# Optimization experiments

Measured on AMD Instinct MI355X. Metric: run time of the kernel, lower is better.

The kernel has to match this reference:

```python
import jax, jax.numpy as jnp
import numpy as np

UNITS = 32
BACKBONE = 64

def lecun_tanh(x):
    return 1.7159 * jnp.tanh(0.666 * x)

def setup_inputs() -> dict:
    key = jax.random.key(0)
    ks = jax.random.split(key, 6)
    B, C, T, H, W = 4, 16, 32, 64, 64
    scale_b = 1.0 / np.sqrt(C + UNITS)
    scale_h = 1.0 / np.sqrt(BACKBONE)
    return {
        "x": jax.random.normal(ks[0], (B, C, T, H, W), jnp.float32),
        "Wb": jax.random.normal(ks[1], (BACKBONE, C + UNITS), jnp.float32) * scale_b,
        "bb": jnp.zeros((BACKBONE,), jnp.float32),
        "Wff1": jax.random.normal(ks[2], (UNITS, BACKBONE), jnp.float32) * scale_h,
        "bff1": jnp.zeros((UNITS,), jnp.float32),
        "Wff2": jax.random.normal(ks[3], (UNITS, BACKBONE), jnp.float32) * scale_h,
        "bff2": jnp.zeros((UNITS,), jnp.float32),
        "Wta": jax.random.normal(ks[4], (UNITS, BACKBONE), jnp.float32) * scale_h,
        "bta": jnp.zeros((UNITS,), jnp.float32),
        "Wtb": jax.random.normal(ks[5], (UNITS, BACKBONE), jnp.float32) * scale_h,
        "btb": jnp.zeros((UNITS,), jnp.float32),
    }

def reference(x, Wb, bb, Wff1, bff1, Wff2, bff2, Wta, bta, Wtb, btb):
    # x: (B, C, T, H, W) -> time-major (T, B, C, H, W) for the scan
    xs = jnp.transpose(x, (2, 0, 1, 3, 4))
    B, C, H, W = x.shape[0], x.shape[1], x.shape[3], x.shape[4]
    h0 = jnp.zeros((B, UNITS, H, W), x.dtype)
    ts = jnp.asarray(1.0, x.dtype)  # no timespans provided -> ts = 1.0

    def head(z, Wh, bh):  # channel-wise (1x1) linear: (B,K,H,W) -> (B,U,H,W)
        return jnp.einsum('bkhw,uk->buhw', z, Wh) + bh[None, :, None, None]

    def step(h, xt):
        z = jnp.concatenate([xt, h], axis=1)  # (B, C+U, H, W)
        z = lecun_tanh(jnp.einsum('bchw,kc->bkhw', z, Wb) + bb[None, :, None, None])
        ff1 = jnp.tanh(head(z, Wff1, bff1))
        ff2 = jnp.tanh(head(z, Wff2, bff2))
        t_a = head(z, Wta, bta)
        t_b = head(z, Wtb, btb)
        t_interp = jax.nn.sigmoid(t_a * ts + t_b)
        h_new = ff1 * (1.0 - t_interp) + t_interp * ff2
        return h_new, h_new

    _, ys = jax.lax.scan(step, h0, xs)  # ys: (T, B, U, H, W)
    # stack along dim=1 (batch_first) then permute(0,2,1,3,4) -> (B, U, T, H, W)
    return jnp.transpose(ys, (1, 2, 0, 3, 4))
```

## Files before the change

### kernel.cpp

```cpp
#include <hip/hip_runtime.h>
#include <hip/hip_bf16.h>


#define CIN      16
#define UNITS    32
#define BACKBONE 64
#define CZ       48
#define TSTEPS   32
#define HW       4096
#define NPIX     16
#define NTHREADS 256
#define KPAD     64

typedef __attribute__((ext_vector_type(8))) short  short8;
typedef __attribute__((ext_vector_type(4))) short  short4v;
typedef __attribute__((ext_vector_type(8))) __bf16 bf16x8;
typedef __attribute__((ext_vector_type(4))) float  float4v;

__device__ __forceinline__ unsigned short bf16_rne(float f) {
    unsigned u = __float_as_uint(f);
    return (unsigned short)((u + 0x7FFFu + ((u >> 16) & 1u)) >> 16);
}
__device__ __forceinline__ float bf16_tof(unsigned short h) {
    return __uint_as_float(((unsigned)h) << 16);
}
__device__ __forceinline__ float tanh_fast(float x) {
    float e = __expf(2.0f * x);
    return 1.0f - __fdividef(2.0f, e + 1.0f);
}
__device__ __forceinline__ float sigmoid_fast(float x) {
    return __fdividef(1.0f, 1.0f + __expf(-x));
}
__device__ __forceinline__ float4v mfma16(bf16x8 a, bf16x8 b, float4v c) {
    return __builtin_amdgcn_mfma_f32_16x16x32_bf16(a, b, c, 0, 0, 0);
}
__device__ __forceinline__ void split8(const float* v, bf16x8& hi, bf16x8& lo) {
    short8 sh, sl;
    #pragma unroll
    for (int j = 0; j < 8; ++j) {
        unsigned short h = bf16_rne(v[j]);
        sh[j] = (short)h;
        sl[j] = (short)bf16_rne(v[j] - bf16_tof(h));
    }
    hi = __builtin_bit_cast(bf16x8, sh);
    lo = __builtin_bit_cast(bf16x8, sl);
}
__device__ __forceinline__ int swoff(int p, int k) {
    return p * KPAD + ((((k >> 3) ^ (p & 7)) << 3) | (k & 7));
}

__global__ __launch_bounds__(NTHREADS, 4)
void cfc_mfma_kernel(const float* __restrict__ x,   const float* __restrict__ Wb,
                     const float* __restrict__ bb,
                     const float* __restrict__ Wff1, const float* __restrict__ bff1,
                     const float* __restrict__ Wff2, const float* __restrict__ bff2,
                     const float* __restrict__ Wta,  const float* __restrict__ bta,
                     const float* __restrict__ Wtb,  const float* __restrict__ btb,
                     float* __restrict__ out)
{
    __shared__ unsigned short zhi[NPIX * KPAD];
    __shared__ unsigned short ahi[NPIX * KPAD];

    const int tid  = threadIdx.x;
    const int wave = tid >> 6;
    const int lane = tid & 63;
    const int ln   = lane & 15;
    const int lq   = lane >> 4;

    const int gpix = blockIdx.x * NPIX;
    const int b    = gpix >> 12;
    const int pinb = gpix & 4095;

    const int mt = wave;
    bf16x8 Abb_hi[2], Abb_lo[2];
    #pragma unroll
    for (int kt = 0; kt < 2; ++kt) {
        float v[8];
        #pragma unroll
        for (int j = 0; j < 8; ++j) {
            int k  = kt * 32 + lq * 8 + j;
            int ki = (k < CZ) ? k : (CZ - 1);
            float raw = Wb[(mt * 16 + ln) * CZ + ki];
            v[j] = (k < CZ) ? raw : 0.0f;
        }
        split8(v, Abb_hi[kt], Abb_lo[kt]);
    }
    const int hsel = ln & 3;
    const float* Whp = (hsel == 0) ? Wff1 : (hsel == 1) ? Wff2 : (hsel == 2) ? Wta : Wtb;
    bf16x8 Ah_hi[2][2], Ah_lo[2][2];
    #pragma unroll
    for (int i = 0; i < 2; ++i) {
        const int u = (wave * 2 + i) * 4 + (ln >> 2);
        #pragma unroll
        for (int kt = 0; kt < 2; ++kt) {
            float v[8];
            #pragma unroll
            for (int j = 0; j < 8; ++j) v[j] = Whp[u * BACKBONE + kt * 32 + lq * 8 + j];
            split8(v, Ah_hi[i][kt], Ah_lo[i][kt]);
        }
    }
    float bbias[4];
    #pragma unroll
    for (int r = 0; r < 4; ++r) bbias[r] = bb[mt * 16 + lq * 4 + r];
    float hbias[2][4];
    #pragma unroll
    for (int i = 0; i < 2; ++i) {
        const int u2 = (wave * 2 + i) * 4 + lq;
        hbias[i][0] = bff1[u2]; hbias[i][1] = bff2[u2];
        hbias[i][2] = bta[u2];  hbias[i][3] = btb[u2];
    }

    for (int i = tid; i < NPIX * KPAD / 2; i += NTHREADS)
        ((unsigned*)zhi)[i] = 0u;
    __syncthreads();
    const int xc = tid >> 4;
    const int xp = tid & 15;
    const float* xb = x + (size_t)(b * CIN + xc) * (TSTEPS * HW) + pinb + xp;
    const int xoff = swoff(xp, xc);
    zhi[xoff] = bf16_rne(xb[0]);

    const int zrd0 = swoff(ln, lq * 8);
    const int zrd1 = swoff(ln, 32 + lq * 8);
    const int awr  = swoff(ln, mt * 16 + lq * 4);
    const int u0   = (wave * 2 + 0) * 4 + lq;
    const int u1   = (wave * 2 + 1) * 4 + lq;
    const int ho0  = swoff(ln, CIN + u0);
    const int ho1  = swoff(ln, CIN + u1);
    float* po0 = out + (size_t)((b * UNITS + u0) * TSTEPS) * HW + pinb + ln;
    float* po1 = out + (size_t)((b * UNITS + u1) * TSTEPS) * HW + pinb + ln;
    int xoffs = HW;
    __syncthreads();

    #pragma unroll 1
    for (int t = 0; t < TSTEPS; ++t) {
        const float xv = xb[xoffs];

        {
            bf16x8 Z0 = __builtin_bit_cast(bf16x8, *(const short8*)&zhi[zrd0]);
            bf16x8 Z1 = __builtin_bit_cast(bf16x8, *(const short8*)&zhi[zrd1]);
            float4v acc = {bbias[0], bbias[1], bbias[2], bbias[3]};
            acc = mfma16(Abb_hi[0], Z0, acc);
            acc = mfma16(Abb_lo[0], Z0, acc);
            acc = mfma16(Abb_hi[1], Z1, acc);
            acc = mfma16(Abb_lo[1], Z1, acc);
            short4v ph;
            #pragma unroll
            for (int r = 0; r < 4; ++r)
                ph[r] = (short)bf16_rne(1.7159f * tanh_fast(0.666f * acc[r]));
            *(short4v*)&ahi[awr] = ph;
        }
        __syncthreads();

        {
            bf16x8 A0 = __builtin_bit_cast(bf16x8, *(const short8*)&ahi[zrd0]);
            bf16x8 A1 = __builtin_bit_cast(bf16x8, *(const short8*)&ahi[zrd1]);

            zhi[xoff] = bf16_rne(xv);

            {
                float4v acc = {hbias[0][0], hbias[0][1], hbias[0][2], hbias[0][3]};
                acc = mfma16(Ah_hi[0][0], A0, acc);
                acc = mfma16(Ah_lo[0][0], A0, acc);
                acc = mfma16(Ah_hi[0][1], A1, acc);
                acc = mfma16(Ah_lo[0][1], A1, acc);
                float f1 = tanh_fast(acc[0]);
                float f2 = tanh_fast(acc[1]);
                float ti = sigmoid_fast(acc[2] + acc[3]);
                float hn = f1 + ti * (f2 - f1);
                *po0 = hn;  po0 += HW;
                zhi[ho0] = bf16_rne(hn);
            }
            {
                float4v acc = {hbias[1][0], hbias[1][1], hbias[1][2], hbias[1][3]};
                acc = mfma16(Ah_hi[1][0], A0, acc);
                acc = mfma16(Ah_lo[1][0], A0, acc);
                acc = mfma16(Ah_hi[1][1], A1, acc);
                acc = mfma16(Ah_lo[1][1], A1, acc);
                float f1 = tanh_fast(acc[0]);
                float f2 = tanh_fast(acc[1]);
                float ti = sigmoid_fast(acc[2] + acc[3]);
                float hn = f1 + ti * (f2 - f1);
                *po1 = hn;  po1 += HW;
                zhi[ho1] = bf16_rne(hn);
            }
        }
        __syncthreads();

        xoffs += (t < TSTEPS - 2) ? HW : 0;
    }
}

extern "C" void kernel_launch(void* const* d_in, const int* in_sizes, int n_in,
                              void* d_out, int out_size, void* d_ws, size_t ws_size,
                              hipStream_t stream) {
    dim3 grid(4 * HW / NPIX);
    cfc_mfma_kernel<<<grid, NTHREADS, 0, stream>>>(
        (const float*)d_in[0], (const float*)d_in[1], (const float*)d_in[2],
        (const float*)d_in[3], (const float*)d_in[4], (const float*)d_in[5],
        (const float*)d_in[6], (const float*)d_in[7], (const float*)d_in[8],
        (const float*)d_in[9], (const float*)d_in[10],
        (float*)d_out);
}
```

Measured before the change: 173.9 us.

## Run each 16-pixel tile in one wave, keep recurrent state in registers

The four-wave block that passed z and backbone activations through shared memory with two barriers per step becomes a single 64-lane wave per block. That wave computes all four backbone M-tiles and all eight head tiles itself. Weight rows are permuted so each MFMA's output lane layout matches the next MFMA's B-operand layout, which lets x, h and the activations move between stages entirely in registers with no LDS and no syncs. It also uses hardware exp2/rcp with packed bf16 conversion and prefetches the next timestep's x. In exchange each wave holds far more weight registers and runs four times the MFMA work serially, and occupancy is set to one block per launch-bounds hint.

```diff
diff --git a/kernel.cpp b/kernel.cpp
--- a/kernel.cpp
+++ b/kernel.cpp
@@ -9,13 +9,12 @@
 #define TSTEPS   32
 #define HW       4096
 #define NPIX     16
-#define NTHREADS 256
-#define KPAD     64
+#define NTHREADS 64
 
 typedef __attribute__((ext_vector_type(8))) short  short8;
-typedef __attribute__((ext_vector_type(4))) short  short4v;
 typedef __attribute__((ext_vector_type(8))) __bf16 bf16x8;
 typedef __attribute__((ext_vector_type(4))) float  float4v;
+typedef __attribute__((ext_vector_type(4))) unsigned int uint4v;
 
 __device__ __forceinline__ unsigned short bf16_rne(float f) {
     unsigned u = __float_as_uint(f);
@@ -24,12 +23,34 @@
 __device__ __forceinline__ float bf16_tof(unsigned short h) {
     return __uint_as_float(((unsigned)h) << 16);
 }
-__device__ __forceinline__ float tanh_fast(float x) {
-    float e = __expf(2.0f * x);
-    return 1.0f - __fdividef(2.0f, e + 1.0f);
-}
-__device__ __forceinline__ float sigmoid_fast(float x) {
-    return __fdividef(1.0f, 1.0f + __expf(-x));
+__device__ __forceinline__ unsigned cvt_pk_bf16(float lo, float hi) {
+    unsigned r;
+    asm("v_cvt_pk_bf16_f32 %0, %1, %2" : "=v"(r) : "v"(lo), "v"(hi));
+    return r;
+}
+
+#if __has_builtin(__builtin_amdgcn_exp2f)
+#define EXP2F(x) __builtin_amdgcn_exp2f(x)
+#else
+#define EXP2F(x) __expf(0.69314718056f * (x))
+#endif
+#if __has_builtin(__builtin_amdgcn_rcpf)
+#define RCPF(x) __builtin_amdgcn_rcpf(x)
+#else
+#define RCPF(x) __fdividef(1.0f, (x))
+#endif
+
+__device__ __forceinline__ float lecun_tanh_f(float v) {
+    float e = EXP2F(1.92166925f * v);
+    return fmaf(-3.4318f, RCPF(e + 1.0f), 1.7159f);
+}
+__device__ __forceinline__ float tanh_f(float v) {
+    float e = EXP2F(2.88539008f * v);
+    return fmaf(-2.0f, RCPF(e + 1.0f), 1.0f);
+}
+__device__ __forceinline__ float sigmoid_f(float v) {
+    float e = EXP2F(-1.44269504f * v);
+    return RCPF(1.0f + e);
 }
 __device__ __forceinline__ float4v mfma16(bf16x8 a, bf16x8 b, float4v c) {
     return __builtin_amdgcn_mfma_f32_16x16x32_bf16(a, b, c, 0, 0, 0);
@@ -45,11 +66,8 @@
     hi = __builtin_bit_cast(bf16x8, sh);
     lo = __builtin_bit_cast(bf16x8, sl);
 }
-__device__ __forceinline__ int swoff(int p, int k) {
-    return p * KPAD + ((((k >> 3) ^ (p & 7)) << 3) | (k & 7));
-}
-
-__global__ __launch_bounds__(NTHREADS, 4)
+
+__global__ __launch_bounds__(NTHREADS, 1)
 void cfc_mfma_kernel(const float* __restrict__ x,   const float* __restrict__ Wb,
                      const float* __restrict__ bb,
                      const float* __restrict__ Wff1, const float* __restrict__ bff1,
@@ -58,135 +76,149 @@
                      const float* __restrict__ Wtb,  const float* __restrict__ btb,
                      float* __restrict__ out)
 {
-    __shared__ unsigned short zhi[NPIX * KPAD];
-    __shared__ unsigned short ahi[NPIX * KPAD];
-
-    const int tid  = threadIdx.x;
-    const int wave = tid >> 6;
-    const int lane = tid & 63;
+    const int lane = threadIdx.x;
     const int ln   = lane & 15;
     const int lq   = lane >> 4;
 
     const int gpix = blockIdx.x * NPIX;
     const int b    = gpix >> 12;
     const int pinb = gpix & 4095;
-
-    const int mt = wave;
-    bf16x8 Abb_hi[2], Abb_lo[2];
-    #pragma unroll
-    for (int kt = 0; kt < 2; ++kt) {
-        float v[8];
-        #pragma unroll
-        for (int j = 0; j < 8; ++j) {
-            int k  = kt * 32 + lq * 8 + j;
-            int ki = (k < CZ) ? k : (CZ - 1);
-            float raw = Wb[(mt * 16 + ln) * CZ + ki];
-            v[j] = (k < CZ) ? raw : 0.0f;
-        }
-        split8(v, Abb_hi[kt], Abb_lo[kt]);
-    }
-    const int hsel = ln & 3;
-    const float* Whp = (hsel == 0) ? Wff1 : (hsel == 1) ? Wff2 : (hsel == 2) ? Wta : Wtb;
-    bf16x8 Ah_hi[2][2], Ah_lo[2][2];
-    #pragma unroll
-    for (int i = 0; i < 2; ++i) {
-        const int u = (wave * 2 + i) * 4 + (ln >> 2);
+    const int px   = pinb + ln;
+
+    bf16x8 Abb_hi[4][2], Abb_lo[4][2];
+    #pragma unroll
+    for (int mt = 0; mt < 4; ++mt) {
         #pragma unroll
         for (int kt = 0; kt < 2; ++kt) {
             float v[8];
             #pragma unroll
-            for (int j = 0; j < 8; ++j) v[j] = Whp[u * BACKBONE + kt * 32 + lq * 8 + j];
+            for (int j = 0; j < 8; ++j) {
+                int c = kt * 32 + lq * 8 + j;
+                v[j] = (c < CZ) ? Wb[(mt * 16 + ln) * CZ + c] : 0.0f;
+            }
+            split8(v, Abb_hi[mt][kt], Abb_lo[mt][kt]);
+        }
+    }
+    float bbias[4][4];
+    #pragma unroll
+    for (int mt = 0; mt < 4; ++mt)
+        #pragma unroll
+        for (int r = 0; r < 4; ++r)
+            bbias[mt][r] = bb[mt * 16 + lq * 4 + r];
+
+    const int head = ln & 3;
+    const float* Whp = (head == 0) ? Wff1 : (head == 1) ? Wff2 : (head == 2) ? Wta : Wtb;
+    const int urow = (((ln >> 2) + 2) & 3) * 8;
+    bf16x8 Ah_hi[8][2], Ah_lo[8][2];
+    #pragma unroll
+    for (int i = 0; i < 8; ++i) {
+        #pragma unroll
+        for (int kt = 0; kt < 2; ++kt) {
+            float v[8];
+            #pragma unroll
+            for (int j = 0; j < 8; ++j) {
+                int n = 32 * kt + (j >> 2) * 16 + lq * 4 + (j & 3);
+                v[j] = Whp[(urow + i) * BACKBONE + n];
+            }
             split8(v, Ah_hi[i][kt], Ah_lo[i][kt]);
         }
     }
-    float bbias[4];
-    #pragma unroll
-    for (int r = 0; r < 4; ++r) bbias[r] = bb[mt * 16 + lq * 4 + r];
-    float hbias[2][4];
-    #pragma unroll
-    for (int i = 0; i < 2; ++i) {
-        const int u2 = (wave * 2 + i) * 4 + lq;
-        hbias[i][0] = bff1[u2]; hbias[i][1] = bff2[u2];
-        hbias[i][2] = bta[u2];  hbias[i][3] = btb[u2];
-    }
-
-    for (int i = tid; i < NPIX * KPAD / 2; i += NTHREADS)
-        ((unsigned*)zhi)[i] = 0u;
-    __syncthreads();
-    const int xc = tid >> 4;
-    const int xp = tid & 15;
-    const float* xb = x + (size_t)(b * CIN + xc) * (TSTEPS * HW) + pinb + xp;
-    const int xoff = swoff(xp, xc);
-    zhi[xoff] = bf16_rne(xb[0]);
-
-    const int zrd0 = swoff(ln, lq * 8);
-    const int zrd1 = swoff(ln, 32 + lq * 8);
-    const int awr  = swoff(ln, mt * 16 + lq * 4);
-    const int u0   = (wave * 2 + 0) * 4 + lq;
-    const int u1   = (wave * 2 + 1) * 4 + lq;
-    const int ho0  = swoff(ln, CIN + u0);
-    const int ho1  = swoff(ln, CIN + u1);
-    float* po0 = out + (size_t)((b * UNITS + u0) * TSTEPS) * HW + pinb + ln;
-    float* po1 = out + (size_t)((b * UNITS + u1) * TSTEPS) * HW + pinb + ln;
-    int xoffs = HW;
-    __syncthreads();
+    const int ub = ((lq + 2) & 3) * 8;
+    float hbias[8][4];
+    #pragma unroll
+    for (int i = 0; i < 8; ++i) {
+        int u = ub + i;
+        hbias[i][0] = bff1[u]; hbias[i][1] = bff2[u];
+        hbias[i][2] = bta[u];  hbias[i][3] = btb[u];
+    }
+
+    const int cb = (lq & 1) * 8;
+    unsigned xo[8], oo[8];
+    #pragma unroll
+    for (int j = 0; j < 8; ++j)
+        xo[j] = (unsigned)(((b * CIN + cb + j) * TSTEPS) * HW + px);
+    #pragma unroll
+    for (int i = 0; i < 8; ++i)
+        oo[i] = (unsigned)(((b * UNITS + ub + i) * TSTEPS) * HW + px);
+
+    float xa[8], xb2[8];
+    #pragma unroll
+    for (int j = 0; j < 8; ++j) xa[j] = x[xo[j]];
+    unsigned hpk[4] = {0u, 0u, 0u, 0u};
+    unsigned toff = 0;
+
+    auto step = [&](int t, float (&xc)[8], float (&xn)[8]) {
+        const unsigned tn = toff + ((t < TSTEPS - 1) ? (unsigned)HW : 0u);
+        #pragma unroll
+        for (int j = 0; j < 8; ++j) xn[j] = x[xo[j] + tn];
+
+        unsigned xpk[4];
+        #pragma unroll
+        for (int p = 0; p < 4; ++p) xpk[p] = cvt_pk_bf16(xc[2 * p], xc[2 * p + 1]);
+        const bool xl = (lq < 2);
+        unsigned z0u[4], z1u[4];
+        #pragma unroll
+        for (int p = 0; p < 4; ++p) {
+            z0u[p] = xl ? xpk[p] : hpk[p];
+            z1u[p] = xl ? hpk[p] : 0u;
+        }
+        uint4v zv0 = {z0u[0], z0u[1], z0u[2], z0u[3]};
+        uint4v zv1 = {z1u[0], z1u[1], z1u[2], z1u[3]};
+        bf16x8 Z0 = __builtin_bit_cast(bf16x8, zv0);
+        bf16x8 Z1 = __builtin_bit_cast(bf16x8, zv1);
+
+        float4v acc[4];
+        #pragma unroll
+        for (int mt = 0; mt < 4; ++mt) {
+            float4v a = {bbias[mt][0], bbias[mt][1], bbias[mt][2], bbias[mt][3]};
+            a = mfma16(Abb_hi[mt][0], Z0, a);
+            a = mfma16(Abb_lo[mt][0], Z0, a);
+            a = mfma16(Abb_hi[mt][1], Z1, a);
+            a = mfma16(Abb_lo[mt][1], Z1, a);
+            acc[mt] = a;
+        }
+
+        bf16x8 A2[2];
+        #pragma unroll
+        for (int kt = 0; kt < 2; ++kt) {
+            unsigned w[4];
+            #pragma unroll
+            for (int h2 = 0; h2 < 2; ++h2) {
+                float g0 = lecun_tanh_f(acc[2 * kt + h2][0]);
+                float g1 = lecun_tanh_f(acc[2 * kt + h2][1]);
+                float g2 = lecun_tanh_f(acc[2 * kt + h2][2]);
+                float g3 = lecun_tanh_f(acc[2 * kt + h2][3]);
+                w[2 * h2 + 0] = cvt_pk_bf16(g0, g1);
+                w[2 * h2 + 1] = cvt_pk_bf16(g2, g3);
+            }
+            uint4v wv = {w[0], w[1], w[2], w[3]};
+            A2[kt] = __builtin_bit_cast(bf16x8, wv);
+        }
+
+        float hn[8];
+        #pragma unroll
+        for (int i = 0; i < 8; ++i) {
+            float4v c = {hbias[i][0], hbias[i][1], hbias[i][2], hbias[i][3]};
+            c = mfma16(Ah_hi[i][0], A2[0], c);
+            c = mfma16(Ah_lo[i][0], A2[0], c);
+            c = mfma16(Ah_hi[i][1], A2[1], c);
+            c = mfma16(Ah_lo[i][1], A2[1], c);
+            float f1 = tanh_f(c[0]);
+            float f2 = tanh_f(c[1]);
+            float ti = sigmoid_f(c[2] + c[3]);
+            float h  = fmaf(ti, f2 - f1, f1);
+            out[oo[i] + toff] = h;
+            hn[i] = h;
+        }
+        #pragma unroll
+        for (int p = 0; p < 4; ++p) hpk[p] = cvt_pk_bf16(hn[2 * p], hn[2 * p + 1]);
+        toff += (unsigned)HW;
+    };
 
     #pragma unroll 1
-    for (int t = 0; t < TSTEPS; ++t) {
-        const float xv = xb[xoffs];
-
-        {
-            bf16x8 Z0 = __builtin_bit_cast(bf16x8, *(const short8*)&zhi[zrd0]);
-            bf16x8 Z1 = __builtin_bit_cast(bf16x8, *(const short8*)&zhi[zrd1]);
-            float4v acc = {bbias[0], bbias[1], bbias[2], bbias[3]};
-            acc = mfma16(Abb_hi[0], Z0, acc);
-            acc = mfma16(Abb_lo[0], Z0, acc);
-            acc = mfma16(Abb_hi[1], Z1, acc);
-            acc = mfma16(Abb_lo[1], Z1, acc);
-            short4v ph;
-            #pragma unroll
-            for (int r = 0; r < 4; ++r)
-                ph[r] = (short)bf16_rne(1.7159f * tanh_fast(0.666f * acc[r]));
-            *(short4v*)&ahi[awr] = ph;
-        }
-        __syncthreads();
-
-        {
-            bf16x8 A0 = __builtin_bit_cast(bf16x8, *(const short8*)&ahi[zrd0]);
-            bf16x8 A1 = __builtin_bit_cast(bf16x8, *(const short8*)&ahi[zrd1]);
-
-            zhi[xoff] = bf16_rne(xv);
-
-            {
-                float4v acc = {hbias[0][0], hbias[0][1], hbias[0][2], hbias[0][3]};
-                acc = mfma16(Ah_hi[0][0], A0, acc);
-                acc = mfma16(Ah_lo[0][0], A0, acc);
-                acc = mfma16(Ah_hi[0][1], A1, acc);
-                acc = mfma16(Ah_lo[0][1], A1, acc);
-                float f1 = tanh_fast(acc[0]);
-                float f2 = tanh_fast(acc[1]);
-                float ti = sigmoid_fast(acc[2] + acc[3]);
-                float hn = f1 + ti * (f2 - f1);
-                *po0 = hn;  po0 += HW;
-                zhi[ho0] = bf16_rne(hn);
-            }
-            {
-                float4v acc = {hbias[1][0], hbias[1][1], hbias[1][2], hbias[1][3]};
-                acc = mfma16(Ah_hi[1][0], A0, acc);
-                acc = mfma16(Ah_lo[1][0], A0, acc);
-                acc = mfma16(Ah_hi[1][1], A1, acc);
-                acc = mfma16(Ah_lo[1][1], A1, acc);
-                float f1 = tanh_fast(acc[0]);
-                float f2 = tanh_fast(acc[1]);
-                float ti = sigmoid_fast(acc[2] + acc[3]);
-                float hn = f1 + ti * (f2 - f1);
-                *po1 = hn;  po1 += HW;
-                zhi[ho1] = bf16_rne(hn);
-            }
-        }
-        __syncthreads();
-
-        xoffs += (t < TSTEPS - 2) ? HW : 0;
+    for (int t = 0; t < TSTEPS; t += 2) {
+        step(t,     xa,  xb2);
+        step(t + 1, xb2, xa);
     }
 }
 
```

Measured after the change: 161.3 us. -7.3%, faster.
